# Performance work log

Hardware: AMD Instinct MI355X
Metric: run time of the kernel (lower is better)

Reference implementation:

```python
import jax, jax.numpy as jnp
import numpy as np

HEADS = 16

def setup_inputs() -> dict:
    key = jax.random.key(0)
    ks = jax.random.split(key, 5)
    dim = 1024
    x = jax.random.normal(ks[0], (2, 2048, dim), dtype=jnp.float32)
    scale = 1.0 / np.sqrt(dim)
    Wq = jax.random.normal(ks[1], (dim, dim), dtype=jnp.float32) * scale
    Wk = jax.random.normal(ks[2], (dim, dim), dtype=jnp.float32) * scale
    Wv = jax.random.normal(ks[3], (dim, dim), dtype=jnp.float32) * scale
    Wo = jax.random.normal(ks[4], (dim, dim), dtype=jnp.float32) * scale
    return {"x": x, "Wq": Wq, "Wk": Wk, "Wv": Wv, "Wo": Wo}

def reference(x, Wq, Wk, Wv, Wo):
    b, n, dim = x.shape
    h = HEADS
    d = dim // h
    # projections: torch Linear y = x @ W.T (W is [out,in])
    def split_heads(t):
        return t.reshape(b, n, h, d).transpose(0, 2, 1, 3)  # b h n d
    q = split_heads(x @ Wq.T)
    k = split_heads(x @ Wk.T)
    v = split_heads(x @ Wv.T)
    scale = jnp.asarray(d, x.dtype) ** -0.5
    dots = jnp.einsum('bhid,bhjd->bhij', q, k) * scale
    # causal mask: positions j > i masked (triu with diagonal 1 since i == j)
    i_idx = jnp.arange(n)[:, None]
    j_idx = jnp.arange(n)[None, :]
    mask_value = -jnp.finfo(dots.dtype).max
    dots = jnp.where(j_idx > i_idx, mask_value, dots)
    attn = jax.nn.softmax(dots, axis=-1)  # dropout p=0 (eval) is identity
    out = jnp.einsum('bhij,bhjd->bhid', attn, v)
    out = out.transpose(0, 2, 1, 3).reshape(b, n, dim)
    return out @ Wo.T
```

## Files before the change

### kernel.cpp

```cpp
#include <hip/hip_runtime.h>
#include <hip/hip_bf16.h>

#define BATCH 2
#define SEQ   2048
#define DIM   1024
#define HEADS 16
#define DIMH  64
#define BK    32
#define LOG2E 1.44269504088896340736f
#define SM_SHIFT 16.0f

typedef __attribute__((ext_vector_type(8))) short short8;
typedef __attribute__((ext_vector_type(4))) short short4v;
typedef __attribute__((ext_vector_type(4))) float floatx4;

static __device__ __forceinline__ void gload_lds16(const void* g, void* l) {
    __builtin_amdgcn_global_load_lds(
        (const __attribute__((address_space(1))) void*)g,
        (__attribute__((address_space(3))) void*)l, 16, 0, 0);
}

static __device__ __forceinline__ unsigned pk_trunc(float a, float b) {
    return (__float_as_uint(b) & 0xffff0000u) | (__float_as_uint(a) >> 16);
}

__global__ __launch_bounds__(256) void conv_all(
    const float* __restrict__ x,  const float* __restrict__ Wq,
    const float* __restrict__ Wk, const float* __restrict__ Wv,
    const float* __restrict__ Wo,
    __hip_bfloat16* __restrict__ dst, __hip_bfloat16* __restrict__ dwo)
{
    const size_t NX = (size_t)BATCH * SEQ * DIM;
    const size_t NW = (size_t)DIM * DIM;
    size_t i = ((size_t)blockIdx.x * 256 + threadIdx.x) * 4;
    if (i >= NX + 4 * NW) return;
    const float* src; __hip_bfloat16* d;
    if (i < NX) { src = x + i; d = dst + i; }
    else if (i < NX + 3 * NW) {
        size_t j = i - NX;
        int w = (int)(j >> 20);
        src = ((w == 0) ? Wq : (w == 1) ? Wk : Wv) + (j & (NW - 1));
        d = dst + i;
    } else {
        size_t off = i - (NX + 3 * NW);
        src = Wo + off; d = dwo + off;
    }
    floatx4 f = *reinterpret_cast<const floatx4*>(src);
    short4v o;
    #pragma unroll
    for (int e = 0; e < 4; ++e) {
        __hip_bfloat16 t = __float2bfloat16(f[e]);
        o[e] = *reinterpret_cast<short*>(&t);
    }
    *reinterpret_cast<short4v*>(d) = o;
}

__global__ __launch_bounds__(256) void gemm_qkv(
    const __hip_bfloat16* __restrict__ xbf,
    const __hip_bfloat16* __restrict__ wbf,
    __hip_bfloat16* __restrict__ qkv)
{
    __shared__ __align__(16) short As[128 * BK];
    __shared__ __align__(16) short Bs[128 * BK];

    const int tid  = threadIdx.x;
    const int wv   = tid >> 6;
    const int lane = tid & 63;
    const int quad = lane >> 4;
    const int l16  = lane & 15;
    const int wm   = wv >> 1, wn = wv & 1;
    const int m0   = blockIdx.x * 128;
    const int n0   = blockIdx.y * 128;
    const int z    = n0 >> 10;
    __hip_bfloat16* out = qkv + (size_t)z * (BATCH * SEQ * DIM);

    const int srow = tid >> 2;
    const int scol = (tid & 3) * 8;

    floatx4 acc[4][4] = {};

    for (int k0 = 0; k0 < DIM; k0 += BK) {
        __syncthreads();
        #pragma unroll
        for (int i = 0; i < 2; ++i) {
            const __hip_bfloat16* ga = xbf + (size_t)(m0 + srow + i * 64) * DIM + k0 + scol;
            const __hip_bfloat16* gb = wbf + (size_t)(n0 + srow + i * 64) * DIM + k0 + scol;
            gload_lds16(ga, (char*)As + i * 4096 + wv * 1024);
            gload_lds16(gb, (char*)Bs + i * 4096 + wv * 1024);
        }
        __syncthreads();

        short8 af[4], bf[4];
        #pragma unroll
        for (int mt = 0; mt < 4; ++mt)
            af[mt] = *reinterpret_cast<const short8*>(&As[(wm * 64 + mt * 16 + l16) * 32 + quad * 8]);
        #pragma unroll
        for (int nt = 0; nt < 4; ++nt)
            bf[nt] = *reinterpret_cast<const short8*>(&Bs[(wn * 64 + nt * 16 + l16) * 32 + quad * 8]);
        #pragma unroll
        for (int mt = 0; mt < 4; ++mt)
            #pragma unroll
            for (int nt = 0; nt < 4; ++nt)
                acc[mt][nt] = __builtin_amdgcn_mfma_f32_16x16x32_bf16(
                    af[mt], bf[nt], acc[mt][nt], 0, 0, 0);
    }

    const float esc = (z == 0) ? (0.125f * LOG2E) : 1.0f;
    #pragma unroll
    for (int mt = 0; mt < 4; ++mt) {
        #pragma unroll
        for (int nt = 0; nt < 4; ++nt) {
            const int n  = n0 + wn * 64 + nt * 16 + l16;
            const int hh = (n >> 6) & 15, dv = n & 63;
            #pragma unroll
            for (int r = 0; r < 4; ++r) {
                const int m  = m0 + wm * 64 + mt * 16 + quad * 4 + r;
                const int bb = m >> 11, nn = m & (SEQ - 1);
                const float v = acc[mt][nt][r] * esc;
                if (z < 2)
                    out[((size_t)(bb * HEADS + hh) * SEQ + nn) * DIMH + dv] = __float2bfloat16(v);
                else
                    out[((size_t)(bb * HEADS + hh) * DIMH + dv) * SEQ + nn] = __float2bfloat16(v);
            }
        }
    }
}

__global__ __launch_bounds__(256) void gemm_out(
    const __hip_bfloat16* __restrict__ qhs,
    const __hip_bfloat16* __restrict__ W,
    float* __restrict__ C)
{
    __shared__ __align__(16) short As[128 * BK];
    __shared__ __align__(16) short Bs[128 * BK];

    const int tid  = threadIdx.x;
    const int wv   = tid >> 6;
    const int lane = tid & 63;
    const int quad = lane >> 4;
    const int l16  = lane & 15;
    const int wm   = wv >> 1, wn = wv & 1;
    const int m0   = blockIdx.x * 128;
    const int n0   = blockIdx.y * 128;

    const int srow = tid >> 2;
    const int scol = (tid & 3) * 8;

    floatx4 acc[4][4] = {};

    for (int k0 = 0; k0 < DIM; k0 += BK) {
        const int h    = k0 >> 6;
        const int koff = k0 & 63;
        __syncthreads();
        #pragma unroll
        for (int i = 0; i < 2; ++i) {
            const int m  = m0 + srow + i * 64;
            const int bb = m >> 11, nn = m & (SEQ - 1);
            gload_lds16(qhs + ((size_t)(bb * HEADS + h) * SEQ + nn) * DIMH + koff + scol,
                        (char*)As + i * 4096 + wv * 1024);
            gload_lds16(W + (size_t)(n0 + srow + i * 64) * DIM + k0 + scol,
                        (char*)Bs + i * 4096 + wv * 1024);
        }
        __syncthreads();

        short8 af[4], bf[4];
        #pragma unroll
        for (int mt = 0; mt < 4; ++mt)
            af[mt] = *reinterpret_cast<const short8*>(&As[(wm * 64 + mt * 16 + l16) * 32 + quad * 8]);
        #pragma unroll
        for (int nt = 0; nt < 4; ++nt)
            bf[nt] = *reinterpret_cast<const short8*>(&Bs[(wn * 64 + nt * 16 + l16) * 32 + quad * 8]);
        #pragma unroll
        for (int mt = 0; mt < 4; ++mt)
            #pragma unroll
            for (int nt = 0; nt < 4; ++nt)
                acc[mt][nt] = __builtin_amdgcn_mfma_f32_16x16x32_bf16(
                    af[mt], bf[nt], acc[mt][nt], 0, 0, 0);
    }

    #pragma unroll
    for (int mt = 0; mt < 4; ++mt)
        #pragma unroll
        for (int nt = 0; nt < 4; ++nt) {
            const int n = n0 + wn * 64 + nt * 16 + l16;
            #pragma unroll
            for (int r = 0; r < 4; ++r) {
                const int m = m0 + wm * 64 + mt * 16 + quad * 4 + r;
                C[(size_t)m * DIM + n] = acc[mt][nt][r];
            }
        }
}

__global__ __launch_bounds__(128) void attn_causal(
    __hip_bfloat16* __restrict__ qkv)
{
    __shared__ __align__(16) short kt[64 * 64];
    __shared__ __align__(16) short vt[64 * 64];
    __shared__ __align__(16) short pt[2][16 * 72];

    const int id    = blockIdx.x;
    const int combo = id & 31;
    const int p     = id >> 5;
    const int b     = combo >> 4;
    const int h     = combo & 15;
    const int tA = p, tB = 63 - p;
    const int nA = (tA + 2) >> 1;
    const int nB = (tB + 2) >> 1;
    const int total = nA + nB;

    const size_t hoff = (size_t)(b * HEADS + h) * SEQ * DIMH;
    const size_t one  = (size_t)BATCH * SEQ * DIM;
    __hip_bfloat16* qb        = qkv + hoff;
    const __hip_bfloat16* kb  = qkv + one + hoff;
    const __hip_bfloat16* vtg = qkv + 2 * one + hoff;

    const int tid  = threadIdx.x;
    const int wv   = tid >> 6;
    const int lane = tid & 63;
    const int quad = lane >> 4;
    const int l16  = lane & 15;
    const int xr   = l16 & 7;

    const short8 kone8 = {0x3F80, 0x3F80, 0x3F80, 0x3F80,
                          0x3F80, 0x3F80, 0x3F80, 0x3F80};

    int q16 = tA * 32 + wv * 16;
    short8 aq0 = *reinterpret_cast<const short8*>(qb + (size_t)(q16 + l16) * DIMH + quad * 8);
    short8 aq1 = *reinterpret_cast<const short8*>(qb + (size_t)(q16 + l16) * DIMH + 32 + quad * 8);
    floatx4 oacc[4] = {};
    floatx4 lsum = {};

    short8 kreg[4], vreg[4];
    #pragma unroll
    for (int i = 0; i < 4; ++i) {
        const int c = tid + 128 * i;
        const int row = c >> 3, jc = c & 7;
        kreg[i] = *reinterpret_cast<const short8*>(kb + (size_t)row * DIMH + jc * 8);
        vreg[i] = *reinterpret_cast<const short8*>(vtg + (size_t)row * SEQ + jc * 8);
    }

    for (int s = 0; s < total; ++s) {
        const bool lastA = (s == nA - 1);
        const int j0 = ((s < nA) ? s : s - nA) * 64;

        __syncthreads();
        #pragma unroll
        for (int i = 0; i < 4; ++i) {
            const int c = tid + 128 * i;
            const int row = c >> 3, jc = c & 7;
            const int off = row * 64 + ((jc ^ (row & 7)) * 8);
            *reinterpret_cast<short8*>(&kt[off]) = kreg[i];
            *reinterpret_cast<short8*>(&vt[off]) = vreg[i];
        }
        __syncthreads();

        if (s + 1 < total) {
            const int s2 = s + 1;
            const int j1 = ((s2 < nA) ? s2 : s2 - nA) * 64;
            #pragma unroll
            for (int i = 0; i < 4; ++i) {
                const int c = tid + 128 * i;
                const int row = c >> 3, jc = c & 7;
                kreg[i] = *reinterpret_cast<const short8*>(kb + (size_t)(j1 + row) * DIMH + jc * 8);
                vreg[i] = *reinterpret_cast<const short8*>(vtg + (size_t)row * SEQ + j1 + jc * 8);
            }
        }

        floatx4 st[4];
        #pragma unroll
        for (int t = 0; t < 4; ++t) {
            const int rw = t * 16 + l16;
            short8 a0 = *reinterpret_cast<const short8*>(&kt[rw * 64 + (quad ^ xr) * 8]);
            short8 a1 = *reinterpret_cast<const short8*>(&kt[rw * 64 + ((quad + 4) ^ xr) * 8]);
            floatx4 zz = {};
            zz    = __builtin_amdgcn_mfma_f32_16x16x32_bf16(a0, aq0, zz, 0, 0, 0);
            st[t] = __builtin_amdgcn_mfma_f32_16x16x32_bf16(a1, aq1, zz, 0, 0, 0);
        }

        if (j0 + 63 > q16) {
            const int qg = q16 + l16;
            #pragma unroll
            for (int t = 0; t < 4; ++t)
                #pragma unroll
                for (int r = 0; r < 4; ++r) {
                    const int jg = j0 + t * 16 + quad * 4 + r;
                    if (jg > qg) st[t][r] = -3.0e38f;
                }
        }

        #pragma unroll
        for (int t = 0; t < 4; ++t)
            #pragma unroll
            for (int r = 0; r < 4; ++r)
                st[t][r] = __builtin_amdgcn_exp2f(st[t][r] - SM_SHIFT);

        #pragma unroll
        for (int t = 0; t < 4; ++t) {
            *reinterpret_cast<unsigned*>(&pt[wv][l16 * 72 + t * 16 + quad * 4]) =
                pk_trunc(st[t][0], st[t][1]);
            *reinterpret_cast<unsigned*>(&pt[wv][l16 * 72 + t * 16 + quad * 4 + 2]) =
                pk_trunc(st[t][2], st[t][3]);
        }
        short8 p0 = *reinterpret_cast<const short8*>(&pt[wv][l16 * 72 + quad * 8]);
        short8 p1 = *reinterpret_cast<const short8*>(&pt[wv][l16 * 72 + 32 + quad * 8]);

        lsum = __builtin_amdgcn_mfma_f32_16x16x32_bf16(kone8, p0, lsum, 0, 0, 0);
        lsum = __builtin_amdgcn_mfma_f32_16x16x32_bf16(kone8, p1, lsum, 0, 0, 0);

        #pragma unroll
        for (int dt = 0; dt < 4; ++dt) {
            const int rw = dt * 16 + l16;
            short8 v0 = *reinterpret_cast<const short8*>(&vt[rw * 64 + (quad ^ xr) * 8]);
            short8 v1 = *reinterpret_cast<const short8*>(&vt[rw * 64 + ((quad + 4) ^ xr) * 8]);
            oacc[dt] = __builtin_amdgcn_mfma_f32_16x16x32_bf16(v0, p0, oacc[dt], 0, 0, 0);
            oacc[dt] = __builtin_amdgcn_mfma_f32_16x16x32_bf16(v1, p1, oacc[dt], 0, 0, 0);
        }

        if (lastA || s == total - 1) {
            const float rl = 1.0f / lsum[0];
            #pragma unroll
            for (int dt = 0; dt < 4; ++dt)
                #pragma unroll
                for (int r = 0; r < 4; ++r)
                    qb[(size_t)(q16 + l16) * DIMH + dt * 16 + quad * 4 + r] =
                        __float2bfloat16(oacc[dt][r] * rl);
            if (lastA) {
                q16 = tB * 32 + wv * 16;
                aq0 = *reinterpret_cast<const short8*>(qb + (size_t)(q16 + l16) * DIMH + quad * 8);
                aq1 = *reinterpret_cast<const short8*>(qb + (size_t)(q16 + l16) * DIMH + 32 + quad * 8);
                #pragma unroll
                for (int dt = 0; dt < 4; ++dt)
                    #pragma unroll
                    for (int r = 0; r < 4; ++r) oacc[dt][r] = 0.f;
                #pragma unroll
                for (int r = 0; r < 4; ++r) lsum[r] = 0.f;
            }
        }
    }
}


extern "C" void kernel_launch(void* const* d_in, const int* in_sizes, int n_in,
                              void* d_out, int out_size, void* d_ws, size_t ws_size,
                              hipStream_t stream) {
    const float* x  = (const float*)d_in[0];
    const float* Wq = (const float*)d_in[1];
    const float* Wk = (const float*)d_in[2];
    const float* Wv = (const float*)d_in[3];
    const float* Wo = (const float*)d_in[4];

    __hip_bfloat16* qkv  = (__hip_bfloat16*)d_ws;
    __hip_bfloat16* wobf = (__hip_bfloat16*)((char*)d_ws + (size_t)24 * 1024 * 1024);

    __hip_bfloat16* xbf = (__hip_bfloat16*)d_out;
    __hip_bfloat16* wbf = xbf + (size_t)BATCH * SEQ * DIM;

    conv_all  <<<8192, 256, 0, stream>>>(x, Wq, Wk, Wv, Wo, xbf, wobf);
    gemm_qkv  <<<dim3((BATCH * SEQ) / 128, (3 * DIM) / 128), 256, 0, stream>>>(xbf, wbf, qkv);
    attn_causal<<<dim3(1024), 128, 0, stream>>>(qkv);
    gemm_out  <<<dim3((BATCH * SEQ) / 128, DIM / 128), 256, 0, stream>>>(qkv, wobf, (float*)d_out);
}
```

Measured before the change: 192.0 us.

## Use single-wave attention blocks with two query tiles per wave, longest-first order

The attention kernel now launches 2048 single-wave blocks of 64 threads instead of 1024 two-wave blocks that each paired a short and a long causal tile. Each wave handles 32 query rows as two 16-row sub-tiles, so every K/V fragment read from LDS feeds twice as many MFMAs, and block-level barriers are no longer needed. Blocks are ordered longest tile first to help load balance. The trade-offs are more register pressure from doubled accumulators and K/V prefetch buffers, and less LDS-staging parallelism per block.

```diff
diff --git a/kernel.cpp b/kernel.cpp
--- a/kernel.cpp
+++ b/kernel.cpp
@@ -13,6 +13,7 @@
 typedef __attribute__((ext_vector_type(8))) short short8;
 typedef __attribute__((ext_vector_type(4))) short short4v;
 typedef __attribute__((ext_vector_type(4))) float floatx4;
+typedef __attribute__((ext_vector_type(2))) unsigned int uint2v;
 
 static __device__ __forceinline__ void gload_lds16(const void* g, void* l) {
     __builtin_amdgcn_global_load_lds(
@@ -191,22 +192,19 @@
         }
 }
 
-__global__ __launch_bounds__(128) void attn_causal(
+__global__ __launch_bounds__(64) void attn_causal(
     __hip_bfloat16* __restrict__ qkv)
 {
     __shared__ __align__(16) short kt[64 * 64];
     __shared__ __align__(16) short vt[64 * 64];
-    __shared__ __align__(16) short pt[2][16 * 72];
+    __shared__ __align__(16) short pt[16 * 72];
 
     const int id    = blockIdx.x;
     const int combo = id & 31;
-    const int p     = id >> 5;
+    const int tile  = 63 - (id >> 5);
     const int b     = combo >> 4;
     const int h     = combo & 15;
-    const int tA = p, tB = 63 - p;
-    const int nA = (tA + 2) >> 1;
-    const int nB = (tB + 2) >> 1;
-    const int total = nA + nB;
+    const int nst   = (tile + 2) >> 1;
 
     const size_t hoff = (size_t)(b * HEADS + h) * SEQ * DIMH;
     const size_t one  = (size_t)BATCH * SEQ * DIM;
@@ -214,9 +212,7 @@
     const __hip_bfloat16* kb  = qkv + one + hoff;
     const __hip_bfloat16* vtg = qkv + 2 * one + hoff;
 
-    const int tid  = threadIdx.x;
-    const int wv   = tid >> 6;
-    const int lane = tid & 63;
+    const int lane = threadIdx.x & 63;
     const int quad = lane >> 4;
     const int l16  = lane & 15;
     const int xr   = l16 & 7;
@@ -224,118 +220,129 @@
     const short8 kone8 = {0x3F80, 0x3F80, 0x3F80, 0x3F80,
                           0x3F80, 0x3F80, 0x3F80, 0x3F80};
 
-    int q16 = tA * 32 + wv * 16;
-    short8 aq0 = *reinterpret_cast<const short8*>(qb + (size_t)(q16 + l16) * DIMH + quad * 8);
-    short8 aq1 = *reinterpret_cast<const short8*>(qb + (size_t)(q16 + l16) * DIMH + 32 + quad * 8);
-    floatx4 oacc[4] = {};
-    floatx4 lsum = {};
-
-    short8 kreg[4], vreg[4];
-    #pragma unroll
-    for (int i = 0; i < 4; ++i) {
-        const int c = tid + 128 * i;
+    const int qbase = tile * 32;
+    short8 aq[2][2];
+    #pragma unroll
+    for (int qt = 0; qt < 2; ++qt) {
+        const __hip_bfloat16* qr = qb + (size_t)(qbase + qt * 16 + l16) * DIMH;
+        aq[qt][0] = *reinterpret_cast<const short8*>(qr + quad * 8);
+        aq[qt][1] = *reinterpret_cast<const short8*>(qr + 32 + quad * 8);
+    }
+    floatx4 oacc[2][4] = {};
+    floatx4 lsum[2] = {};
+
+    short8 kreg[8], vreg[8];
+    #pragma unroll
+    for (int u = 0; u < 8; ++u) {
+        const int c = lane + 64 * u;
         const int row = c >> 3, jc = c & 7;
-        kreg[i] = *reinterpret_cast<const short8*>(kb + (size_t)row * DIMH + jc * 8);
-        vreg[i] = *reinterpret_cast<const short8*>(vtg + (size_t)row * SEQ + jc * 8);
-    }
-
-    for (int s = 0; s < total; ++s) {
-        const bool lastA = (s == nA - 1);
-        const int j0 = ((s < nA) ? s : s - nA) * 64;
-
-        __syncthreads();
-        #pragma unroll
-        for (int i = 0; i < 4; ++i) {
-            const int c = tid + 128 * i;
+        kreg[u] = *reinterpret_cast<const short8*>(kb + (size_t)row * DIMH + jc * 8);
+        vreg[u] = *reinterpret_cast<const short8*>(vtg + (size_t)row * SEQ + jc * 8);
+    }
+
+    for (int s = 0; s < nst; ++s) {
+        const int j0 = s * 64;
+
+        #pragma unroll
+        for (int u = 0; u < 8; ++u) {
+            const int c = lane + 64 * u;
             const int row = c >> 3, jc = c & 7;
             const int off = row * 64 + ((jc ^ (row & 7)) * 8);
-            *reinterpret_cast<short8*>(&kt[off]) = kreg[i];
-            *reinterpret_cast<short8*>(&vt[off]) = vreg[i];
-        }
-        __syncthreads();
-
-        if (s + 1 < total) {
-            const int s2 = s + 1;
-            const int j1 = ((s2 < nA) ? s2 : s2 - nA) * 64;
-            #pragma unroll
-            for (int i = 0; i < 4; ++i) {
-                const int c = tid + 128 * i;
+            *reinterpret_cast<short8*>(&kt[off]) = kreg[u];
+            *reinterpret_cast<short8*>(&vt[off]) = vreg[u];
+        }
+
+        if (s + 1 < nst) {
+            const int j1 = j0 + 64;
+            #pragma unroll
+            for (int u = 0; u < 8; ++u) {
+                const int c = lane + 64 * u;
                 const int row = c >> 3, jc = c & 7;
-                kreg[i] = *reinterpret_cast<const short8*>(kb + (size_t)(j1 + row) * DIMH + jc * 8);
-                vreg[i] = *reinterpret_cast<const short8*>(vtg + (size_t)row * SEQ + j1 + jc * 8);
-            }
-        }
-
-        floatx4 st[4];
+                kreg[u] = *reinterpret_cast<const short8*>(kb + (size_t)(j1 + row) * DIMH + jc * 8);
+                vreg[u] = *reinterpret_cast<const short8*>(vtg + (size_t)row * SEQ + j1 + jc * 8);
+            }
+        }
+
+        short8 ka0[4], ka1[4];
         #pragma unroll
         for (int t = 0; t < 4; ++t) {
             const int rw = t * 16 + l16;
-            short8 a0 = *reinterpret_cast<const short8*>(&kt[rw * 64 + (quad ^ xr) * 8]);
-            short8 a1 = *reinterpret_cast<const short8*>(&kt[rw * 64 + ((quad + 4) ^ xr) * 8]);
-            floatx4 zz = {};
-            zz    = __builtin_amdgcn_mfma_f32_16x16x32_bf16(a0, aq0, zz, 0, 0, 0);
-            st[t] = __builtin_amdgcn_mfma_f32_16x16x32_bf16(a1, aq1, zz, 0, 0, 0);
-        }
-
-        if (j0 + 63 > q16) {
-            const int qg = q16 + l16;
+            ka0[t] = *reinterpret_cast<const short8*>(&kt[rw * 64 + (quad ^ xr) * 8]);
+            ka1[t] = *reinterpret_cast<const short8*>(&kt[rw * 64 + ((quad + 4) ^ xr) * 8]);
+        }
+
+        floatx4 st[2][4];
+        #pragma unroll
+        for (int qt = 0; qt < 2; ++qt)
+            #pragma unroll
+            for (int t = 0; t < 4; ++t) {
+                floatx4 zz = {};
+                zz        = __builtin_amdgcn_mfma_f32_16x16x32_bf16(ka0[t], aq[qt][0], zz, 0, 0, 0);
+                st[qt][t] = __builtin_amdgcn_mfma_f32_16x16x32_bf16(ka1[t], aq[qt][1], zz, 0, 0, 0);
+            }
+
+        #pragma unroll
+        for (int qt = 0; qt < 2; ++qt) {
+            const int q16 = qbase + qt * 16;
+            if (j0 + 63 > q16) {
+                const int qg = q16 + l16;
+                #pragma unroll
+                for (int t = 0; t < 4; ++t)
+                    #pragma unroll
+                    for (int r = 0; r < 4; ++r) {
+                        const int jg = j0 + t * 16 + quad * 4 + r;
+                        if (jg > qg) st[qt][t][r] = -3.0e38f;
+                    }
+            }
+        }
+
+        #pragma unroll
+        for (int qt = 0; qt < 2; ++qt)
             #pragma unroll
             for (int t = 0; t < 4; ++t)
                 #pragma unroll
-                for (int r = 0; r < 4; ++r) {
-                    const int jg = j0 + t * 16 + quad * 4 + r;
-                    if (jg > qg) st[t][r] = -3.0e38f;
-                }
-        }
-
-        #pragma unroll
-        for (int t = 0; t < 4; ++t)
-            #pragma unroll
-            for (int r = 0; r < 4; ++r)
-                st[t][r] = __builtin_amdgcn_exp2f(st[t][r] - SM_SHIFT);
-
-        #pragma unroll
-        for (int t = 0; t < 4; ++t) {
-            *reinterpret_cast<unsigned*>(&pt[wv][l16 * 72 + t * 16 + quad * 4]) =
-                pk_trunc(st[t][0], st[t][1]);
-            *reinterpret_cast<unsigned*>(&pt[wv][l16 * 72 + t * 16 + quad * 4 + 2]) =
-                pk_trunc(st[t][2], st[t][3]);
-        }
-        short8 p0 = *reinterpret_cast<const short8*>(&pt[wv][l16 * 72 + quad * 8]);
-        short8 p1 = *reinterpret_cast<const short8*>(&pt[wv][l16 * 72 + 32 + quad * 8]);
-
-        lsum = __builtin_amdgcn_mfma_f32_16x16x32_bf16(kone8, p0, lsum, 0, 0, 0);
-        lsum = __builtin_amdgcn_mfma_f32_16x16x32_bf16(kone8, p1, lsum, 0, 0, 0);
-
+                for (int r = 0; r < 4; ++r)
+                    st[qt][t][r] = __builtin_amdgcn_exp2f(st[qt][t][r] - SM_SHIFT);
+
+        short8 vf0[4], vf1[4];
         #pragma unroll
         for (int dt = 0; dt < 4; ++dt) {
             const int rw = dt * 16 + l16;
-            short8 v0 = *reinterpret_cast<const short8*>(&vt[rw * 64 + (quad ^ xr) * 8]);
-            short8 v1 = *reinterpret_cast<const short8*>(&vt[rw * 64 + ((quad + 4) ^ xr) * 8]);
-            oacc[dt] = __builtin_amdgcn_mfma_f32_16x16x32_bf16(v0, p0, oacc[dt], 0, 0, 0);
-            oacc[dt] = __builtin_amdgcn_mfma_f32_16x16x32_bf16(v1, p1, oacc[dt], 0, 0, 0);
-        }
-
-        if (lastA || s == total - 1) {
-            const float rl = 1.0f / lsum[0];
-            #pragma unroll
-            for (int dt = 0; dt < 4; ++dt)
-                #pragma unroll
-                for (int r = 0; r < 4; ++r)
-                    qb[(size_t)(q16 + l16) * DIMH + dt * 16 + quad * 4 + r] =
-                        __float2bfloat16(oacc[dt][r] * rl);
-            if (lastA) {
-                q16 = tB * 32 + wv * 16;
-                aq0 = *reinterpret_cast<const short8*>(qb + (size_t)(q16 + l16) * DIMH + quad * 8);
-                aq1 = *reinterpret_cast<const short8*>(qb + (size_t)(q16 + l16) * DIMH + 32 + quad * 8);
-                #pragma unroll
-                for (int dt = 0; dt < 4; ++dt)
-                    #pragma unroll
-                    for (int r = 0; r < 4; ++r) oacc[dt][r] = 0.f;
-                #pragma unroll
-                for (int r = 0; r < 4; ++r) lsum[r] = 0.f;
-            }
-        }
+            vf0[dt] = *reinterpret_cast<const short8*>(&vt[rw * 64 + (quad ^ xr) * 8]);
+            vf1[dt] = *reinterpret_cast<const short8*>(&vt[rw * 64 + ((quad + 4) ^ xr) * 8]);
+        }
+
+        #pragma unroll
+        for (int qt = 0; qt < 2; ++qt) {
+            #pragma unroll
+            for (int t = 0; t < 4; ++t) {
+                uint2v u2 = { pk_trunc(st[qt][t][0], st[qt][t][1]),
+                              pk_trunc(st[qt][t][2], st[qt][t][3]) };
+                *reinterpret_cast<uint2v*>(&pt[l16 * 72 + t * 16 + quad * 4]) = u2;
+            }
+            short8 p0 = *reinterpret_cast<const short8*>(&pt[l16 * 72 + quad * 8]);
+            short8 p1 = *reinterpret_cast<const short8*>(&pt[l16 * 72 + 32 + quad * 8]);
+
+            lsum[qt] = __builtin_amdgcn_mfma_f32_16x16x32_bf16(kone8, p0, lsum[qt], 0, 0, 0);
+            lsum[qt] = __builtin_amdgcn_mfma_f32_16x16x32_bf16(kone8, p1, lsum[qt], 0, 0, 0);
+
+            #pragma unroll
+            for (int dt = 0; dt < 4; ++dt) {
+                oacc[qt][dt] = __builtin_amdgcn_mfma_f32_16x16x32_bf16(vf0[dt], p0, oacc[qt][dt], 0, 0, 0);
+                oacc[qt][dt] = __builtin_amdgcn_mfma_f32_16x16x32_bf16(vf1[dt], p1, oacc[qt][dt], 0, 0, 0);
+            }
+        }
+    }
+
+    #pragma unroll
+    for (int qt = 0; qt < 2; ++qt) {
+        const float rl = 1.0f / lsum[qt][0];
+        __hip_bfloat16* orow = qb + (size_t)(qbase + qt * 16 + l16) * DIMH;
+        #pragma unroll
+        for (int dt = 0; dt < 4; ++dt)
+            #pragma unroll
+            for (int r = 0; r < 4; ++r)
+                orow[dt * 16 + quad * 4 + r] = __float2bfloat16(oacc[qt][dt][r] * rl);
     }
 }
 
@@ -357,6 +364,6 @@
 
     conv_all  <<<8192, 256, 0, stream>>>(x, Wq, Wk, Wv, Wo, xbf, wobf);
     gemm_qkv  <<<dim3((BATCH * SEQ) / 128, (3 * DIM) / 128), 256, 0, stream>>>(xbf, wbf, qkv);
-    attn_causal<<<dim3(1024), 128, 0, stream>>>(qkv);
+    attn_causal<<<dim3(2048), 64, 0, stream>>>(qkv);
     gemm_out  <<<dim3((BATCH * SEQ) / 128, DIM / 128), 256, 0, stream>>>(qkv, wobf, (float*)d_out);
 }
```

After: 193.5 us. Within noise of the previous version (+0.8%).
